# Performance work log

Hardware: AMD Instinct MI355X
Metric: run time of the kernel (lower is better)

The kernel has to match this reference:

```python
import jax, jax.numpy as jnp
import numpy as np

BETA = 0.25          # commitment loss weight (init kwarg)
CODEBOOK_SIZE = 2048


def setup_inputs() -> dict:
    key = jax.random.key(0)
    k1, k2 = jax.random.split(key)
    B, L, D = 8, 4096, 256
    z_e = jax.random.normal(k1, (B, L, D), dtype=jnp.float32)
    # xavier_uniform-style init for the codebook
    limit = float(np.sqrt(6.0 / (CODEBOOK_SIZE + D)))
    embed_weight = jax.random.uniform(k2, (CODEBOOK_SIZE, D), dtype=jnp.float32,
                                      minval=-limit, maxval=limit)
    return {"z_e": z_e, "embed_weight": embed_weight}


def reference(z_e, embed_weight):
    # eval-mode forward (no EMA buffer updates)
    B, L, D = z_e.shape
    K = embed_weight.shape[0]
    zf = z_e.reshape(-1, D)                                   # [N, D]
    d2 = (jnp.sum(zf * zf, axis=1, keepdims=True)
          - 2.0 * (zf @ embed_weight.T)
          + jnp.sum(embed_weight * embed_weight, axis=1)[None, :])
    distances = jnp.sqrt(jnp.maximum(d2, 0.0))                # [N, K]
    idx = jnp.argmin(distances, axis=1)                       # [N]
    z_q = embed_weight[idx].reshape(B, L, D)                  # gather

    commitment_loss = BETA * jnp.mean((jax.lax.stop_gradient(z_q) - z_e) ** 2)
    embedding_loss = jnp.mean((jax.lax.stop_gradient(z_e) - z_q) ** 2)

    # avg over one-hot encodings == normalized histogram of idx
    N = zf.shape[0]
    counts = jax.ops.segment_sum(jnp.ones((N,), jnp.float32), idx, num_segments=K)
    avg_probs = counts / N
    perplexity = jnp.exp(-jnp.sum(avg_probs * jnp.log(avg_probs + 1e-10)))
    vq_loss = commitment_loss + embedding_loss - 0.01 * perplexity

    z_q_st = z_e + jax.lax.stop_gradient(z_q - z_e)           # straight-through
    return z_q_st, vq_loss, idx.reshape(B, L)
```

## Files before the change

### kernel.cpp

```cpp
#include <hip/hip_runtime.h>
#include <math.h>

#define DDIM 256
#define NSPLIT 4
#define TILES_PER_SPLIT 16
#define TILE_CODES 32
#define TILE_BYTES 16384
#define SMEM_BYTES 32768

typedef __attribute__((ext_vector_type(8))) short short8v;
typedef __attribute__((ext_vector_type(4))) float float4v;
typedef unsigned int u32;
typedef unsigned short u16;

__device__ __forceinline__ short f2bf(float x) {
    u32 u = __float_as_uint(x);
    u = u + 0x7fffu + ((u >> 16) & 1u);
    return (short)(u >> 16);
}

__device__ __forceinline__ void gload_lds16(const void* g, void* l) {
    __builtin_amdgcn_global_load_lds(
        (const __attribute__((address_space(1))) u32*)g,
        (__attribute__((address_space(3))) u32*)l, 16, 0, 0);
}

__device__ __forceinline__ float np_sq_chain(const float* v, int lane) {
    #pragma clang fp contract(off)
    const int half = lane >> 3, j = lane & 7;
    const float* base = v + half * 128 + j;
    float x = base[0];
    float c = x * x;
    #pragma unroll
    for (int m = 1; m < 16; ++m) {
        float y = base[8 * m];
        float s = y * y;
        c = c + s;
    }
    return c;
}

__device__ __forceinline__ float np_combine16(const float* c) {
    #pragma clang fp contract(off)
    float L = ((c[0] + c[1]) + (c[2] + c[3])) + ((c[4] + c[5]) + (c[6] + c[7]));
    float R = ((c[8] + c[9]) + (c[10] + c[11])) + ((c[12] + c[13]) + (c[14] + c[15]));
    return L + R;
}

__device__ __forceinline__ void ins3(float m, int k,
                                     float& v0, float& v1, float& v2,
                                     int& i0, int& i1, int& i2) {
    if (m < v0)      { v2 = v1; i2 = i1; v1 = v0; i1 = i0; v0 = m; i0 = k; }
    else if (m < v1) { v2 = v1; i2 = i1; v1 = m;  i1 = k; }
    else if (m < v2) { v2 = m;  i2 = k; }
}

__global__ void zero_counts_kernel(int* __restrict__ counts, int K) {
    int i = blockIdx.x * 256 + threadIdx.x;
    if (i < K) counts[i] = 0;
}

__global__ void code_norms_np_kernel(const float* __restrict__ e, float* __restrict__ e2) {
    __shared__ float buf[DDIM];
    __shared__ float ch[16];
    int k = blockIdx.x;
    int t = threadIdx.x;
    float4 v = *(const float4*)&e[(size_t)k * DDIM + t * 4];
    *(float4*)&buf[t * 4] = v;
    __syncthreads();
    if (t < 16) ch[t] = np_sq_chain(buf, t);
    __syncthreads();
    if (t == 0) e2[k] = np_combine16(ch);
}

__global__ void convert_permute_e_kernel(const float* __restrict__ e, char* __restrict__ ebf_p) {
    int id = blockIdx.x * 256 + threadIdx.x;
    int k = id >> 5, d8 = id & 31;
    const float* s = &e[(size_t)k * DDIM + d8 * 8];
    float4 f0 = *(const float4*)s;
    float4 f1 = *(const float4*)(s + 4);
    short8v v;
    v[0] = f2bf(f0.x); v[1] = f2bf(f0.y); v[2] = f2bf(f0.z); v[3] = f2bf(f0.w);
    v[4] = f2bf(f1.x); v[5] = f2bf(f1.y); v[6] = f2bf(f1.z); v[7] = f2bf(f1.w);
    *(short8v*)(ebf_p + ((size_t)(k >> 5) << 14) + d8 * 512 + (k & 31) * 16) = v;
}

__global__ __launch_bounds__(256, 2)
void vq_cand_kernel(const float* __restrict__ z, const char* __restrict__ ebf_p,
                    const float* __restrict__ e2, u16* __restrict__ cand) {
    extern __shared__ char smem[];
    const int t    = threadIdx.x;
    const int w    = t >> 6;
    const int lane = t & 63;
    const int quad = lane >> 4;
    const int l15  = lane & 15;
    const int s    = blockIdx.y;
    const int row0 = blockIdx.x * 256;
    const int rw0  = row0 + w * 64;

    short8v zf[4][8];
    #pragma unroll
    for (int j = 0; j < 4; ++j) {
        const float* zr = &z[(size_t)(rw0 + j * 16 + l15) * DDIM];
        #pragma unroll
        for (int kk = 0; kk < 8; ++kk) {
            int d0 = kk * 32 + quad * 8;
            float4 f0 = *(const float4*)&zr[d0];
            float4 f1 = *(const float4*)&zr[d0 + 4];
            short8v v;
            v[0] = f2bf(f0.x); v[1] = f2bf(f0.y); v[2] = f2bf(f0.z); v[3] = f2bf(f0.w);
            v[4] = f2bf(f1.x); v[5] = f2bf(f1.y); v[6] = f2bf(f1.z); v[7] = f2bf(f1.w);
            zf[j][kk] = v;
        }
    }

    float v0[4], v1[4], v2[4];
    int   i0[4], i1[4], i2[4];
    #pragma unroll
    for (int j = 0; j < 4; ++j) {
        v0[j] = 3.4e38f; v1[j] = 3.4e38f; v2[j] = 3.4e38f;
        i0[j] = 0x7fff;  i1[j] = 0x7fff;  i2[j] = 0x7fff;
    }

    const char* tile_base = ebf_p + (size_t)s * TILES_PER_SPLIT * TILE_BYTES;

    {
        const char* src = tile_base + w * 4096 + lane * 16;
        char* dst = smem + w * 4096;
        #pragma unroll
        for (int q = 0; q < 4; ++q) gload_lds16(src + q * 1024, dst + q * 1024);
    }
    __syncthreads();

    #pragma unroll 1
    for (int tt = 0; tt < TILES_PER_SPLIT; ++tt) {
        if (tt + 1 < TILES_PER_SPLIT) {
            const char* src = tile_base + (size_t)(tt + 1) * TILE_BYTES + w * 4096 + lane * 16;
            char* dst = smem + ((tt + 1) & 1) * TILE_BYTES + w * 4096;
            #pragma unroll
            for (int q = 0; q < 4; ++q) gload_lds16(src + q * 1024, dst + q * 1024);
        }
        const short* es = (const short*)(smem + (tt & 1) * TILE_BYTES);

        float4v acc[2][4];
        #pragma unroll
        for (int i = 0; i < 2; ++i)
            #pragma unroll
            for (int j = 0; j < 4; ++j) acc[i][j] = (float4v)0.0f;

        #pragma unroll
        for (int kk = 0; kk < 8; ++kk) {
            int c = kk * 4 + quad;
            short8v a0 = *(const short8v*)&es[c * 256 + l15 * 8];
            short8v a1 = *(const short8v*)&es[c * 256 + (16 + l15) * 8];
            #pragma unroll
            for (int j = 0; j < 4; ++j) {
                acc[0][j] = __builtin_amdgcn_mfma_f32_16x16x32_bf16(a0, zf[j][kk], acc[0][j], 0, 0, 0);
                acc[1][j] = __builtin_amdgcn_mfma_f32_16x16x32_bf16(a1, zf[j][kk], acc[1][j], 0, 0, 0);
            }
        }

        const int kbase = s * 512 + tt * TILE_CODES;
        #pragma unroll
        for (int i = 0; i < 2; ++i) {
            #pragma unroll
            for (int reg = 0; reg < 4; ++reg) {
                int cl = i * 16 + quad * 4 + reg;
                float ev = e2[kbase + cl];
                int   kc = kbase + cl;
                #pragma unroll
                for (int j = 0; j < 4; ++j) {
                    float m = fmaf(-2.0f, acc[i][j][reg], ev);
                    ins3(m, kc, v0[j], v1[j], v2[j], i0[j], i1[j], i2[j]);
                }
            }
        }
        __syncthreads();
    }

    float* mv = (float*)smem;
    short* mi = (short*)(smem + 12288);
    #pragma unroll
    for (int j = 0; j < 4; ++j) {
        int rl = w * 64 + j * 16 + l15;
        int sl = quad * 3;
        mv[rl * 12 + sl]     = v0[j];  mi[rl * 12 + sl]     = (short)i0[j];
        mv[rl * 12 + sl + 1] = v1[j];  mi[rl * 12 + sl + 1] = (short)i1[j];
        mv[rl * 12 + sl + 2] = v2[j];  mi[rl * 12 + sl + 2] = (short)i2[j];
    }
    __syncthreads();
    {
        float bv0 = 3.4e38f, bv1 = 3.4e38f, bv2 = 3.4e38f;
        int   bi0 = 0x7fff,  bi1 = 0x7fff,  bi2 = 0x7fff;
        for (int x = 0; x < 12; ++x) {
            float m  = mv[t * 12 + x];
            int   k2 = (int)mi[t * 12 + x];
            if (m < bv0 || (m == bv0 && k2 < bi0)) {
                bv2 = bv1; bi2 = bi1; bv1 = bv0; bi1 = bi0; bv0 = m; bi0 = k2;
            } else if (m < bv1 || (m == bv1 && k2 < bi1)) {
                bv2 = bv1; bi2 = bi1; bv1 = m; bi1 = k2;
            } else if (m < bv2 || (m == bv2 && k2 < bi2)) {
                bv2 = m; bi2 = k2;
            }
        }
        u16* cp = &cand[(size_t)(row0 + t) * 12 + s * 3];
        cp[0] = (u16)bi0; cp[1] = (u16)bi1; cp[2] = (u16)bi2;
    }
}

__global__ void refine_fused_kernel(const float* __restrict__ z, const float* __restrict__ e,
                                    const float* __restrict__ e2np, const u16* __restrict__ cand,
                                    int* __restrict__ counts, float* __restrict__ partials,
                                    float* __restrict__ out_zq, float* __restrict__ out_idx) {
    __shared__ float buf[4][DDIM];
    __shared__ float ch[4][16];
    __shared__ float wsum[4];
    const int w = threadIdx.x >> 6;
    const int t = threadIdx.x & 63;
    const int n = blockIdx.x * 4 + w;

    float4 zv = *(const float4*)&z[(size_t)n * DDIM + t * 4];
    *(float4*)&buf[w][t * 4] = zv;
    __syncthreads();
    if (t < 16) ch[w][t] = np_sq_chain(buf[w], t);
    __syncthreads();

    float dotf[12];
    int   kc[12];
    #pragma unroll
    for (int c = 0; c < 12; ++c) {
        int k = cand[(size_t)n * 12 + c];
        kc[c] = k;
        float4 ev = *(const float4*)&e[(size_t)k * DDIM + t * 4];
        double p = (double)zv.x * (double)ev.x + (double)zv.y * (double)ev.y
                 + (double)zv.z * (double)ev.z + (double)zv.w * (double)ev.w;
        #pragma unroll
        for (int o = 32; o > 0; o >>= 1) p += __shfl_down(p, o);
        dotf[c] = (float)p;
    }

    int bk = 0;
    if (t == 0) {
        #pragma clang fp contract(off)
        float sx = np_combine16(ch[w]);
        float bd = 3.4e38f;
        bk = 0x7fffffff;
        #pragma unroll
        for (int c = 0; c < 12; ++c) {
            float twod = 2.0f * dotf[c];
            float t1 = sx - twod;
            float d2v = t1 + e2np[kc[c]];
            d2v = fmaxf(d2v, 0.0f);
            float d = sqrtf(d2v);
            if (d < bd || (d == bd && kc[c] < bk)) { bd = d; bk = kc[c]; }
        }
    }
    int wk = __shfl(bk, 0);

    float4 ev = *(const float4*)&e[(size_t)wk * DDIM + t * 4];
    *(float4*)&out_zq[(size_t)n * DDIM + t * 4] = ev;
    float dx = zv.x - ev.x, dy = zv.y - ev.y, dz = zv.z - ev.z, dw = zv.w - ev.w;
    float sq = dx * dx + dy * dy + dz * dz + dw * dw;
    #pragma unroll
    for (int o = 32; o > 0; o >>= 1) sq += __shfl_down(sq, o);
    if (t == 0) {
        wsum[w] = sq;
        atomicAdd(&counts[wk], 1);
        out_idx[n] = (float)wk;
    }
    __syncthreads();
    if (threadIdx.x == 0)
        partials[blockIdx.x] = wsum[0] + wsum[1] + wsum[2] + wsum[3];
}

__global__ void finalize_kernel(const int* __restrict__ counts, const float* __restrict__ partials,
                                float* __restrict__ out_loss, int K, int NB,
                                float invN, float invND) {
    int t = threadIdx.x;
    double ent = 0.0, sq = 0.0;
    for (int k = t; k < K; k += 256) {
        float p = (float)counts[k] * invN;
        ent += (double)(p * logf(p + 1e-10f));
    }
    for (int i = t; i < NB; i += 256) sq += (double)partials[i];
    #pragma unroll
    for (int o = 32; o > 0; o >>= 1) {
        ent += __shfl_down(ent, o);
        sq  += __shfl_down(sq, o);
    }
    __shared__ double e4[4], s4[4];
    if ((t & 63) == 0) { e4[t >> 6] = ent; s4[t >> 6] = sq; }
    __syncthreads();
    if (t == 0) {
        double esum = e4[0] + e4[1] + e4[2] + e4[3];
        double ssum = s4[0] + s4[1] + s4[2] + s4[3];
        float perp = expf((float)(-esum));
        float mean = (float)ssum * invND;
        out_loss[0] = 1.25f * mean - 0.01f * perp;
    }
}

extern "C" void kernel_launch(void* const* d_in, const int* in_sizes, int n_in,
                              void* d_out, int out_size, void* d_ws, size_t ws_size,
                              hipStream_t stream) {
    const float* z = (const float*)d_in[0];
    const float* e = (const float*)d_in[1];
    const int N = in_sizes[0] / DDIM;
    const int K = in_sizes[1] / DDIM;

    float* out      = (float*)d_out;
    float* out_zq   = out;
    float* out_loss = out + (size_t)N * DDIM;
    float* out_idx  = out_loss + 1;

    int*   counts   = (int*)d_ws;
    float* e2np     = (float*)((char*)d_ws + 8192);
    float* partials = (float*)((char*)d_ws + 16384);
    u16*   cand     = (u16*)((char*)d_ws + 49152);
    char*  ebf_p    = (char*)d_ws + 835584;

    zero_counts_kernel<<<(K + 255) / 256, 256, 0, stream>>>(counts, K);
    code_norms_np_kernel<<<K, 64, 0, stream>>>(e, e2np);
    convert_permute_e_kernel<<<K * 32 / 256, 256, 0, stream>>>(e, ebf_p);
    vq_cand_kernel<<<dim3(N / 256, NSPLIT), 256, SMEM_BYTES, stream>>>(z, ebf_p, e2np, cand);
    refine_fused_kernel<<<N / 4, 256, 0, stream>>>(z, e, e2np, cand, counts, partials,
                                                   out_zq, out_idx);
    finalize_kernel<<<1, 256, 0, stream>>>(counts, partials, out_loss, K, N / 4,
                                           1.0f / (float)N, 1.0f / (float)(N * DDIM));
}
```

Before: 495.1 us.

## Halve rows per block, shuffle-merge top-3, and refine only best six candidates

The candidate kernel now handles 128 rows per block (32 per wave) and requests 3 waves per SIMD in its launch bounds, aiming for more parallelism and occupancy. The cross-quad top-3 merge now uses wave shuffles instead of an LDS round trip, and the approximate distances are written out next to the indices. The refine kernel uses those distances to keep only the 6 best of 12 candidates before the exact fp64 dot products, halving gathers and reductions. The risk is that a true nearest code outside the bf16 top-6 is now missed, and the extra float distance array adds memory traffic.

```diff
diff --git a/kernel.cpp b/kernel.cpp
--- a/kernel.cpp
+++ b/kernel.cpp
@@ -6,7 +6,6 @@
 #define TILES_PER_SPLIT 16
 #define TILE_CODES 32
 #define TILE_BYTES 16384
-#define SMEM_BYTES 32768
 
 typedef __attribute__((ext_vector_type(8))) short short8v;
 typedef __attribute__((ext_vector_type(4))) float float4v;
@@ -85,22 +84,32 @@
     *(short8v*)(ebf_p + ((size_t)(k >> 5) << 14) + d8 * 512 + (k & 31) * 16) = v;
 }
 
-__global__ __launch_bounds__(256, 2)
+__global__ __launch_bounds__(256, 3)
 void vq_cand_kernel(const float* __restrict__ z, const char* __restrict__ ebf_p,
-                    const float* __restrict__ e2, u16* __restrict__ cand) {
-    extern __shared__ char smem[];
+                    const float* __restrict__ e2, float* __restrict__ cand_v,
+                    u16* __restrict__ cand_i) {
+    __shared__ char smem[2][TILE_BYTES];
     const int t    = threadIdx.x;
     const int w    = t >> 6;
     const int lane = t & 63;
     const int quad = lane >> 4;
     const int l15  = lane & 15;
     const int s    = blockIdx.y;
-    const int row0 = blockIdx.x * 256;
-    const int rw0  = row0 + w * 64;
-
-    short8v zf[4][8];
-    #pragma unroll
-    for (int j = 0; j < 4; ++j) {
+    const int row0 = blockIdx.x * 128;
+    const int rw0  = row0 + w * 32;
+
+    const char* tile_base = ebf_p + (size_t)s * TILES_PER_SPLIT * TILE_BYTES;
+
+    {
+        const char* src = tile_base + w * 4096 + lane * 16;
+        char* dst = smem[0] + w * 4096;
+        #pragma unroll
+        for (int q = 0; q < 4; ++q) gload_lds16(src + q * 1024, dst + q * 1024);
+    }
+
+    short8v zf[2][8];
+    #pragma unroll
+    for (int j = 0; j < 2; ++j) {
         const float* zr = &z[(size_t)(rw0 + j * 16 + l15) * DDIM];
         #pragma unroll
         for (int kk = 0; kk < 8; ++kk) {
@@ -114,50 +123,41 @@
         }
     }
 
-    float v0[4], v1[4], v2[4];
-    int   i0[4], i1[4], i2[4];
-    #pragma unroll
-    for (int j = 0; j < 4; ++j) {
+    float v0[2], v1[2], v2[2];
+    int   i0[2], i1[2], i2[2];
+    #pragma unroll
+    for (int j = 0; j < 2; ++j) {
         v0[j] = 3.4e38f; v1[j] = 3.4e38f; v2[j] = 3.4e38f;
         i0[j] = 0x7fff;  i1[j] = 0x7fff;  i2[j] = 0x7fff;
     }
 
-    const char* tile_base = ebf_p + (size_t)s * TILES_PER_SPLIT * TILE_BYTES;
-
-    {
-        const char* src = tile_base + w * 4096 + lane * 16;
-        char* dst = smem + w * 4096;
-        #pragma unroll
-        for (int q = 0; q < 4; ++q) gload_lds16(src + q * 1024, dst + q * 1024);
-    }
     __syncthreads();
 
     #pragma unroll 1
     for (int tt = 0; tt < TILES_PER_SPLIT; ++tt) {
         if (tt + 1 < TILES_PER_SPLIT) {
             const char* src = tile_base + (size_t)(tt + 1) * TILE_BYTES + w * 4096 + lane * 16;
-            char* dst = smem + ((tt + 1) & 1) * TILE_BYTES + w * 4096;
+            char* dst = smem[(tt + 1) & 1] + w * 4096;
             #pragma unroll
             for (int q = 0; q < 4; ++q) gload_lds16(src + q * 1024, dst + q * 1024);
         }
-        const short* es = (const short*)(smem + (tt & 1) * TILE_BYTES);
-
-        float4v acc[2][4];
+        const char* es = smem[tt & 1];
+
+        float4v acc[2][2];
         #pragma unroll
         for (int i = 0; i < 2; ++i)
             #pragma unroll
-            for (int j = 0; j < 4; ++j) acc[i][j] = (float4v)0.0f;
+            for (int j = 0; j < 2; ++j) acc[i][j] = (float4v)0.0f;
 
         #pragma unroll
         for (int kk = 0; kk < 8; ++kk) {
             int c = kk * 4 + quad;
-            short8v a0 = *(const short8v*)&es[c * 256 + l15 * 8];
-            short8v a1 = *(const short8v*)&es[c * 256 + (16 + l15) * 8];
-            #pragma unroll
-            for (int j = 0; j < 4; ++j) {
-                acc[0][j] = __builtin_amdgcn_mfma_f32_16x16x32_bf16(a0, zf[j][kk], acc[0][j], 0, 0, 0);
-                acc[1][j] = __builtin_amdgcn_mfma_f32_16x16x32_bf16(a1, zf[j][kk], acc[1][j], 0, 0, 0);
-            }
+            short8v a0 = *(const short8v*)(es + c * 512 + l15 * 16);
+            short8v a1 = *(const short8v*)(es + c * 512 + (16 + l15) * 16);
+            acc[0][0] = __builtin_amdgcn_mfma_f32_16x16x32_bf16(a0, zf[0][kk], acc[0][0], 0, 0, 0);
+            acc[0][1] = __builtin_amdgcn_mfma_f32_16x16x32_bf16(a0, zf[1][kk], acc[0][1], 0, 0, 0);
+            acc[1][0] = __builtin_amdgcn_mfma_f32_16x16x32_bf16(a1, zf[0][kk], acc[1][0], 0, 0, 0);
+            acc[1][1] = __builtin_amdgcn_mfma_f32_16x16x32_bf16(a1, zf[1][kk], acc[1][1], 0, 0, 0);
         }
 
         const int kbase = s * 512 + tt * TILE_CODES;
@@ -169,7 +169,7 @@
                 float ev = e2[kbase + cl];
                 int   kc = kbase + cl;
                 #pragma unroll
-                for (int j = 0; j < 4; ++j) {
+                for (int j = 0; j < 2; ++j) {
                     float m = fmaf(-2.0f, acc[i][j][reg], ev);
                     ins3(m, kc, v0[j], v1[j], v2[j], i0[j], i1[j], i2[j]);
                 }
@@ -178,38 +178,33 @@
         __syncthreads();
     }
 
-    float* mv = (float*)smem;
-    short* mi = (short*)(smem + 12288);
-    #pragma unroll
-    for (int j = 0; j < 4; ++j) {
-        int rl = w * 64 + j * 16 + l15;
-        int sl = quad * 3;
-        mv[rl * 12 + sl]     = v0[j];  mi[rl * 12 + sl]     = (short)i0[j];
-        mv[rl * 12 + sl + 1] = v1[j];  mi[rl * 12 + sl + 1] = (short)i1[j];
-        mv[rl * 12 + sl + 2] = v2[j];  mi[rl * 12 + sl + 2] = (short)i2[j];
-    }
-    __syncthreads();
-    {
-        float bv0 = 3.4e38f, bv1 = 3.4e38f, bv2 = 3.4e38f;
-        int   bi0 = 0x7fff,  bi1 = 0x7fff,  bi2 = 0x7fff;
-        for (int x = 0; x < 12; ++x) {
-            float m  = mv[t * 12 + x];
-            int   k2 = (int)mi[t * 12 + x];
-            if (m < bv0 || (m == bv0 && k2 < bi0)) {
-                bv2 = bv1; bi2 = bi1; bv1 = bv0; bi1 = bi0; bv0 = m; bi0 = k2;
-            } else if (m < bv1 || (m == bv1 && k2 < bi1)) {
-                bv2 = bv1; bi2 = bi1; bv1 = m; bi1 = k2;
-            } else if (m < bv2 || (m == bv2 && k2 < bi2)) {
-                bv2 = m; bi2 = k2;
-            }
-        }
-        u16* cp = &cand[(size_t)(row0 + t) * 12 + s * 3];
-        cp[0] = (u16)bi0; cp[1] = (u16)bi1; cp[2] = (u16)bi2;
+    #pragma unroll
+    for (int j = 0; j < 2; ++j) {
+        float bm0 = 3.4e38f, bm1 = 3.4e38f, bm2 = 3.4e38f;
+        int   bk0 = 0x7fff,  bk1 = 0x7fff,  bk2 = 0x7fff;
+        #pragma unroll
+        for (int q = 0; q < 4; ++q) {
+            int src = l15 + q * 16;
+            float m0 = __shfl(v0[j], src); int k0 = __shfl(i0[j], src);
+            float m1 = __shfl(v1[j], src); int k1 = __shfl(i1[j], src);
+            float m2 = __shfl(v2[j], src); int k2 = __shfl(i2[j], src);
+            ins3(m0, k0, bm0, bm1, bm2, bk0, bk1, bk2);
+            ins3(m1, k1, bm0, bm1, bm2, bk0, bk1, bk2);
+            ins3(m2, k2, bm0, bm1, bm2, bk0, bk1, bk2);
+        }
+        if (quad == 0) {
+            size_t base = (size_t)(rw0 + j * 16 + l15) * 12 + s * 3;
+            cand_v[base]     = bm0;  cand_i[base]     = (u16)bk0;
+            cand_v[base + 1] = bm1;  cand_i[base + 1] = (u16)bk1;
+            cand_v[base + 2] = bm2;  cand_i[base + 2] = (u16)bk2;
+        }
     }
 }
 
 __global__ void refine_fused_kernel(const float* __restrict__ z, const float* __restrict__ e,
-                                    const float* __restrict__ e2np, const u16* __restrict__ cand,
+                                    const float* __restrict__ e2np,
+                                    const float* __restrict__ cand_v,
+                                    const u16* __restrict__ cand_i,
                                     int* __restrict__ counts, float* __restrict__ partials,
                                     float* __restrict__ out_zq, float* __restrict__ out_idx) {
     __shared__ float buf[4][DDIM];
@@ -225,12 +220,27 @@
     if (t < 16) ch[w][t] = np_sq_chain(buf[w], t);
     __syncthreads();
 
-    float dotf[12];
-    int   kc[12];
+    float bv[6]; int bi[6];
+    #pragma unroll
+    for (int c = 0; c < 6; ++c) { bv[c] = 3.4e38f; bi[c] = 0x7fffffff; }
     #pragma unroll
     for (int c = 0; c < 12; ++c) {
-        int k = cand[(size_t)n * 12 + c];
-        kc[c] = k;
+        float v  = cand_v[(size_t)n * 12 + c];
+        int   id = (int)cand_i[(size_t)n * 12 + c];
+        #pragma unroll
+        for (int x = 0; x < 6; ++x) {
+            if (v < bv[x] || (v == bv[x] && id < bi[x])) {
+                for (int d = 5; d > x; --d) { bv[d] = bv[d - 1]; bi[d] = bi[d - 1]; }
+                bv[x] = v; bi[x] = id;
+                break;
+            }
+        }
+    }
+
+    float dotf[6];
+    #pragma unroll
+    for (int c = 0; c < 6; ++c) {
+        int k = bi[c];
         float4 ev = *(const float4*)&e[(size_t)k * DDIM + t * 4];
         double p = (double)zv.x * (double)ev.x + (double)zv.y * (double)ev.y
                  + (double)zv.z * (double)ev.z + (double)zv.w * (double)ev.w;
@@ -246,13 +256,13 @@
         float bd = 3.4e38f;
         bk = 0x7fffffff;
         #pragma unroll
-        for (int c = 0; c < 12; ++c) {
+        for (int c = 0; c < 6; ++c) {
             float twod = 2.0f * dotf[c];
             float t1 = sx - twod;
-            float d2v = t1 + e2np[kc[c]];
+            float d2v = t1 + e2np[bi[c]];
             d2v = fmaxf(d2v, 0.0f);
             float d = sqrtf(d2v);
-            if (d < bd || (d == bd && kc[c] < bk)) { bd = d; bk = kc[c]; }
+            if (d < bd || (d == bd && bi[c] < bk)) { bd = d; bk = bi[c]; }
         }
     }
     int wk = __shfl(bk, 0);
@@ -316,15 +326,16 @@
     int*   counts   = (int*)d_ws;
     float* e2np     = (float*)((char*)d_ws + 8192);
     float* partials = (float*)((char*)d_ws + 16384);
-    u16*   cand     = (u16*)((char*)d_ws + 49152);
-    char*  ebf_p    = (char*)d_ws + 835584;
+    float* cand_v   = (float*)((char*)d_ws + 49152);
+    u16*   cand_i   = (u16*)((char*)d_ws + 1622016);
+    char*  ebf_p    = (char*)d_ws + 2408448;
 
     zero_counts_kernel<<<(K + 255) / 256, 256, 0, stream>>>(counts, K);
     code_norms_np_kernel<<<K, 64, 0, stream>>>(e, e2np);
     convert_permute_e_kernel<<<K * 32 / 256, 256, 0, stream>>>(e, ebf_p);
-    vq_cand_kernel<<<dim3(N / 256, NSPLIT), 256, SMEM_BYTES, stream>>>(z, ebf_p, e2np, cand);
-    refine_fused_kernel<<<N / 4, 256, 0, stream>>>(z, e, e2np, cand, counts, partials,
-                                                   out_zq, out_idx);
+    vq_cand_kernel<<<dim3(N / 128, NSPLIT), 256, 0, stream>>>(z, ebf_p, e2np, cand_v, cand_i);
+    refine_fused_kernel<<<N / 4, 256, 0, stream>>>(z, e, e2np, cand_v, cand_i,
+                                                   counts, partials, out_zq, out_idx);
     finalize_kernel<<<1, 256, 0, stream>>>(counts, partials, out_loss, K, N / 4,
                                            1.0f / (float)N, 1.0f / (float)(N * DDIM));
 }
```

After: 552.1 us. +11.5%, slower.
